# Optimization experiments

Hardware: AMD Instinct MI355X
Metric: run time of the kernel (lower is better)

## Reference

```python
import jax, jax.numpy as jnp
import numpy as np

V, B, NP, NJ = 5, 32, 20, 17
NB = 16
ND = 128
POSE_MIN_DEPTH, POSE_MAX_DEPTH = 2000.0, 8000.0
POSE_SIGMA = 100.0
KS = 11
HIDDEN_ROUGH, HIDDEN = 1024, 1024
BONES = np.array([[0,1],[0,2],[1,3],[2,4],[5,6],[5,7],[7,9],[6,8],[8,10],[5,11],[6,12],[11,12],[11,13],[13,15],[12,14],[14,16]], dtype=np.int32)


def setup_inputs() -> dict:
    key = jax.random.key(0)
    ks = jax.random.split(key, 12)
    wh = jnp.array([1920.0, 1080.0], jnp.float32)
    kpts = jax.random.uniform(ks[0], (V, B, NP, NJ, 2), jnp.float32) * wh
    pose_vis = jnp.ones((V, B, NP), jnp.float32)
    joint_vis = (jax.random.uniform(ks[1], (V, B, NP, NJ)) > 0.15).astype(jnp.float32)
    gt_pose_depths = jax.random.uniform(ks[2], (B, NP), jnp.float32, 2000.0, 8000.0)
    gt_joint_depths = jax.random.uniform(ks[3], (B, NP, NJ), jnp.float32, -100.0, 100.0)
    angles = np.linspace(-0.3, 0.3, V)
    Rs = np.stack([np.array([[np.cos(a), 0.0, np.sin(a)], [0.0, 1.0, 0.0], [-np.sin(a), 0.0, np.cos(a)]], dtype=np.float32) for a in angles])
    cam_R = jnp.broadcast_to(jnp.asarray(Rs)[:, None], (V, B, 3, 3))
    tvec = np.zeros((V, 3), np.float32); tvec[:, 0] = np.linspace(-500.0, 500.0, V)
    cam_T = jnp.broadcast_to(jnp.asarray(tvec)[:, None], (V, B, 3))
    cam_f = jnp.full((V, B, 2), 1400.0, jnp.float32)
    cam_c = jnp.broadcast_to(jnp.array([960.0, 540.0], jnp.float32), (V, B, 2))
    image_wh = jnp.broadcast_to(jnp.array([1920.0, 1080.0], jnp.float32), (V, B, 2))
    num_persons = jax.random.randint(ks[4], (V, B), 10, NP + 1, jnp.int32)
    Wr1 = jax.random.normal(ks[5], (HIDDEN_ROUGH, NJ * 2)) * 0.02
    br1 = jnp.zeros((HIDDEN_ROUGH,), jnp.float32)
    Wr2 = jax.random.normal(ks[6], (NJ, HIDDEN_ROUGH)) * 0.02
    br2 = jnp.zeros((NJ,), jnp.float32)
    Wc1 = jax.random.normal(ks[7], (HIDDEN, NJ + NB, 3)) * 0.02
    bc1 = jnp.zeros((HIDDEN,), jnp.float32)
    Wc2 = jax.random.normal(ks[8], (1, HIDDEN, 3)) * 0.02
    bc2 = jnp.zeros((1,), jnp.float32)
    bones = jnp.asarray(BONES)
    return dict(kpts=kpts, pose_vis=pose_vis, joint_vis=joint_vis, gt_pose_depths=gt_pose_depths, gt_joint_depths=gt_joint_depths, cam_R=cam_R, cam_T=cam_T, cam_f=cam_f, cam_c=cam_c, image_wh=image_wh, num_persons=num_persons, Wr1=Wr1, br1=br1, Wr2=Wr2, br2=br2, Wc1=Wc1, bc1=bc1, Wc2=Wc2, bc2=bc2, bones=bones)


def _bone_len(p, bones):
    # p: [B, Np, Nj, D, 2] -> [B, Np, Nb, D]
    a = p[:, :, bones[:, 0]]
    b = p[:, :, bones[:, 1]]
    return jnp.sqrt(jnp.sum((a - b) ** 2, -1) + 1e-12)


def _conv1d(x, w, b):
    # x [N,C,L], w [O,I,3]
    y = jax.lax.conv_general_dilated(x, w, (1,), 'SAME', dimension_numbers=('NCH', 'OIH', 'NCH'))
    return y + b[None, :, None]


def _forward(kpts, joint_vis, cam_R, cam_T, cam_f, cam_c, image_wh, num_persons, Wr1, br1, Wr2, br2, Wc1, bc1, Wc2, bc2, bones):
    V_, B_, NP_, NJ_, _ = kpts.shape
    labels = jnp.arange(ND, dtype=jnp.float32) / (ND - 1) * (POSE_MAX_DEPTH - POSE_MIN_DEPTH) + POSE_MIN_DEPTH
    kt = kpts[0]  # target-view 2D poses [B,Np,Nj,2]
    # faithful to original indexing quirk: normalize all batches by batch-0 image size
    kn = kt / image_wh[0, 0][None, None, None, :]
    x = kn.reshape(B_ * NP_, NJ_ * 2)
    h = jax.nn.relu(x @ Wr1.T + br1)
    rough = (h @ Wr2.T + br2).reshape(B_, NP_, NJ_) * 1000.0
    rough = jax.lax.stop_gradient(rough)  # .detach() in original
    depths = labels[None, None, None, :] + rough[..., None]  # [B,Np,Nj,D]
    # back-project target 2D poses at every depth hypothesis
    R0, T0, f0, c0 = cam_R[0], cam_T[0], cam_f[0], cam_c[0]
    uvn = (kt - c0[:, None, None, :]) / f0[:, None, None, :]
    xy = uvn[..., None, :] * depths[..., None]
    cam_pts = jnp.concatenate([xy, depths[..., None]], -1)
    p3d = jnp.einsum('bji,bpkdj->bpkdi', R0, cam_pts) + T0[:, None, None, None, :]  # world [B,Np,Nj,D,3]

    scores = scores2 = boundings = boundings2 = None
    for rv in range(1, V_):
        Rr, Tr, fr, cr = cam_R[rv], cam_T[rv], cam_f[rv], cam_c[rv]
        xc = jnp.einsum('bij,bpkdj->bpkdi', Rr, p3d - Tr[:, None, None, None, :])
        p2t = xc[..., :2] / (xc[..., 2:3] + 1e-8) * fr[:, None, None, None, :] + cr[:, None, None, None, :]
        pr = kpts[rv]         # [B,Npr,Nj,2]
        vr = joint_vis[rv]    # [B,Npr,Nj]
        # pairwise dist over (target-person, ref-person) per joint/depth
        d = jnp.sum((p2t[:, :, None] - pr[:, None, :, :, None, :]) ** 2, -1)  # [B,Npt,Npr,Nj,D]
        w = vr[:, None, :, :, None]
        pdist = jnp.sum(d * w, 3) / (jnp.sum(w, 3) + 1e-8)  # [B,Npt,Npr,D]
        valid = jnp.arange(NP_)[None, None, :, None] < num_persons[rv][:, None, None, None]
        pdist = jnp.where(valid, pdist, 1e5)
        mm = jnp.argmin(pdist, 2)  # [B,Npt,D] nearest ref pose
        bidx = jnp.arange(B_)[:, None, None]
        matched = jnp.transpose(pr[bidx, mm], (0, 1, 3, 2, 4))  # [B,Npt,Nj,D,2]
        mvis = jnp.transpose(vr[bidx, mm], (0, 1, 3, 2))        # [B,Npt,Nj,D]
        mdist = jnp.sum((p2t - matched) ** 2, -1)
        score = jnp.exp(-jnp.sqrt(mdist + 1e-12) / POSE_SIGMA)  # panoptic branch
        score_bl = jnp.exp(-jnp.abs(_bone_len(matched, bones) - _bone_len(p2t, bones)) / 5.0)
        wimg = image_wh[rv][:, None, None, None, 0]
        himg = image_wh[rv][:, None, None, None, 1]
        inb = ((p2t[..., 0] >= 0) & (p2t[..., 1] >= 0) & (p2t[..., 0] <= wimg - 1) & (p2t[..., 1] <= himg - 1)).astype(score.dtype)
        bounding = inb * mvis
        bounding2 = jnp.broadcast_to(mvis[:, :, :1, :], score_bl.shape)
        if scores is None:
            scores, scores2 = score * bounding, score_bl * bounding2
            boundings, boundings2 = bounding, bounding2
        else:
            scores = scores + score * bounding
            scores2 = scores2 + score_bl * bounding2
            boundings = boundings + bounding
            boundings2 = boundings2 + bounding2
    psv = (scores / (boundings + 1e-8)).reshape(B_ * NP_, NJ_, ND)
    psv2 = (scores2 / (boundings2 + 1e-8)).reshape(B_ * NP_, NB, ND)
    xin = jnp.concatenate([psv, psv2], 1)  # [BN, Nj+Nb, D]
    hc = jax.nn.relu(_conv1d(xin, Wc1, bc1))
    logits = _conv1d(hc, Wc2, bc2)[:, 0, :]  # [BN, D]
    vol = jax.nn.softmax(logits, -1)
    # soft-argmax restricted to a window around the argmax
    pos = jnp.arange(ND, dtype=vol.dtype)
    idx = jnp.argmax(vol, -1)
    mask = (jnp.abs(pos[None, :] - idx[:, None].astype(vol.dtype)) <= KS // 2).astype(vol.dtype)
    mv = vol * mask
    mv = mv / (jnp.sum(mv, -1, keepdims=True) + 1e-8)
    pred_idx = jnp.sum(mv * pos, -1).reshape(B_, NP_)
    return pred_idx / (ND - 1) * (POSE_MAX_DEPTH - POSE_MIN_DEPTH) + POSE_MIN_DEPTH


def reference(kpts, pose_vis, joint_vis, gt_pose_depths, gt_joint_depths, cam_R, cam_T, cam_f, cam_c, image_wh, num_persons, Wr1, br1, Wr2, br2, Wc1, bc1, Wc2, bc2, bones):
    return _forward(kpts, joint_vis, cam_R, cam_T, cam_f, cam_c, image_wh, num_persons, Wr1, br1, Wr2, br2, Wc1, bc1, Wc2, bc2, bones)
```

## Files before the change

kernel.cpp:

```cpp
#include <hip/hip_runtime.h>
#include <math.h>

#define VV  5
#define BB  32
#define NPP 20
#define NJJ 17
#define NBB 16
#define NDD 128
#define HID 1024
#define KPITCH 128
#define KSTEPS 7
#define PRP 36
#define VRP 20

typedef __attribute__((ext_vector_type(8))) short short8;
typedef __attribute__((ext_vector_type(16))) float float16;

static constexpr int BONE_A[NBB] = {0,0,1,2,5,5,7,6,8,5,6,11,11,13,12,14};
static constexpr int BONE_B[NBB] = {1,2,3,4,6,7,9,8,10,11,12,12,13,15,14,16};

__device__ __forceinline__ float warp_red_sum(float v) {
#pragma unroll
  for (int off = 32; off >= 1; off >>= 1) v += __shfl_xor(v, off, 64);
  return v;
}

__global__ __launch_bounds__(256) void prep_kernel(
    const float* __restrict__ Wc1, unsigned short* __restrict__ A_hi,
    unsigned short* __restrict__ A_lo) {
  int idx = blockIdx.x * 256 + threadIdx.x;
  int o = idx >> 7, kk = idx & 127;
  float x = (kk < 99) ? Wc1[o * 99 + kk] : 0.0f;
  unsigned int u = __float_as_uint(x);
  unsigned short hi = (unsigned short)(u >> 16);
  float xh = __uint_as_float((u >> 16) << 16);
  float r = x - xh;
  unsigned short lo = (unsigned short)(__float_as_uint(r) >> 16);
  A_hi[idx] = hi;
  A_lo[idx] = lo;
}

__global__ __launch_bounds__(512, 8) void pose_front_kernel(
    const float* __restrict__ kpts, const float* __restrict__ joint_vis,
    const float* __restrict__ cam_R, const float* __restrict__ cam_T,
    const float* __restrict__ cam_f, const float* __restrict__ cam_c,
    const float* __restrict__ image_wh, const int* __restrict__ num_persons,
    const float* __restrict__ Wr1, const float* __restrict__ br1,
    const float* __restrict__ Wr2, const float* __restrict__ br2,
    float* __restrict__ ws_xin) {
  const int n = blockIdx.x;
  const int b = n / NPP;
  const int p = n % NPP;
  const int tid = threadIdx.x;
  const int wv = tid >> 6, ln = tid & 63;
  const int rvv = tid >> 7;
  const int d   = tid & (NDD - 1);

  __shared__ float sh_x[NJJ * 2];
  __shared__ float sh_h[HID];
  __shared__ float sh_rough[NJJ];
  __shared__ float sh_base[NJJ][3];
  __shared__ __align__(16) float sh_pr[4][NPP][PRP];
  __shared__ __align__(16) float sh_vr[4][NPP][VRP];
  __shared__ float sh_stage[4][8][NDD];
  __shared__ float sh_s2red[NBB][NDD];

  if (tid < NJJ * 2) {
    int j = tid >> 1, c = tid & 1;
    float k = kpts[((size_t)(b * NPP + p)) * NJJ * 2 + j * 2 + c];
    sh_x[tid] = k / image_wh[c];
  }
  __syncthreads();

#pragma unroll
  for (int k = 0; k < 2; ++k) {
    int m = tid + k * 512;
    float acc = br1[m];
#pragma unroll
    for (int c = 0; c < NJJ * 2; ++c) acc = fmaf(Wr1[m * (NJJ * 2) + c], sh_x[c], acc);
    sh_h[m] = fmaxf(acc, 0.0f);
  }
  __syncthreads();

  for (int j = wv; j < NJJ; j += 8) {
    float part = 0.0f;
    for (int m = ln; m < HID; m += 64) part = fmaf(Wr2[j * HID + m], sh_h[m], part);
    part = warp_red_sum(part);
    if (ln == 0) sh_rough[j] = (part + br2[j]) * 1000.0f;
  }
  if (tid < NJJ) {
    int j = tid;
    const float* R0 = cam_R + (size_t)b * 9;
    float c0x = cam_c[b * 2 + 0], c0y = cam_c[b * 2 + 1];
    float f0x = cam_f[b * 2 + 0], f0y = cam_f[b * 2 + 1];
    float kx = kpts[((size_t)(b * NPP + p)) * NJJ * 2 + j * 2 + 0];
    float ky = kpts[((size_t)(b * NPP + p)) * NJJ * 2 + j * 2 + 1];
    float ux = (kx - c0x) / f0x;
    float uy = (ky - c0y) / f0y;
#pragma unroll
    for (int i = 0; i < 3; ++i)
      sh_base[j][i] = R0[0 * 3 + i] * ux + R0[1 * 3 + i] * uy + R0[2 * 3 + i];
  }
#pragma unroll
  for (int rr = 0; rr < 4; ++rr) {
    const float* prg = kpts + ((size_t)(rr + 1) * BB + b) * NPP * NJJ * 2;
    for (int idx = tid; idx < NPP * NJJ * 2; idx += 512)
      sh_pr[rr][idx / 34][idx % 34] = prg[idx];
    const float* vrg = joint_vis + ((size_t)(rr + 1) * BB + b) * NPP * NJJ;
    for (int idx = tid; idx < NPP * NJJ; idx += 512)
      sh_vr[rr][idx / 17][idx % 17] = vrg[idx];
  }
  if (tid < 4 * BB) {
    int rr = tid >> 5, q = tid & 31;
    if (q < NPP) {
      sh_pr[rr][q][34] = 0.0f; sh_pr[rr][q][35] = 0.0f;
      sh_vr[rr][q][17] = 0.0f; sh_vr[rr][q][18] = 0.0f; sh_vr[rr][q][19] = 0.0f;
    }
  }
  __syncthreads();

  float partA[NJJ];
  float partS[NBB];
  unsigned int maskB;
  float partb2;
  {
    const int rv = rvv + 1;
    const int vb = rv * BB + b;
    const float* Rr = cam_R + (size_t)vb * 9;
    const float R00 = Rr[0], R01 = Rr[1], R02 = Rr[2];
    const float R10 = Rr[3], R11 = Rr[4], R12 = Rr[5];
    const float R20 = Rr[6], R21 = Rr[7], R22 = Rr[8];
    const float Trx = cam_T[vb * 3 + 0], Try = cam_T[vb * 3 + 1], Trz = cam_T[vb * 3 + 2];
    const float frx = cam_f[vb * 2 + 0], fry = cam_f[vb * 2 + 1];
    const float crx = cam_c[vb * 2 + 0], cry = cam_c[vb * 2 + 1];
    const float wmax = image_wh[vb * 2 + 0] - 1.0f;
    const float hmax = image_wh[vb * 2 + 1] - 1.0f;
    const int nprv = num_persons[vb];
    const float T0x = cam_T[b * 3 + 0], T0y = cam_T[b * 3 + 1], T0z = cam_T[b * 3 + 2];
    const float lab = ((float)d / 127.0f) * 6000.0f + 2000.0f;

    float px[NJJ], py[NJJ];
#pragma unroll
    for (int j = 0; j < NJJ; ++j) {
      float dep = lab + sh_rough[j];
      float p0 = fmaf(dep, sh_base[j][0], T0x);
      float p1 = fmaf(dep, sh_base[j][1], T0y);
      float p2 = fmaf(dep, sh_base[j][2], T0z);
      float q0 = p0 - Trx, q1 = p1 - Try, q2 = p2 - Trz;
      float xc0 = R00 * q0 + R01 * q1 + R02 * q2;
      float xc1 = R10 * q0 + R11 * q1 + R12 * q2;
      float xc2 = R20 * q0 + R21 * q1 + R22 * q2 + 1e-8f;
      px[j] = xc0 / xc2 * frx + crx;
      py[j] = xc1 / xc2 * fry + cry;
    }

    float best = 3.4e38f;
    int mm = 0;
#pragma unroll 1
    for (int q = 0; q < NPP; ++q) {
      const float4* pr4 = (const float4*)(&sh_pr[rvv][q][0]);
      const float4* vr4 = (const float4*)(&sh_vr[rvv][q][0]);
      float num = 0.0f, den = 0.0f;
#pragma unroll
      for (int g4 = 0; g4 < 4; ++g4) {
        float4 w  = vr4[g4];
        float4 pa = pr4[2 * g4 + 0];
        float4 pb = pr4[2 * g4 + 1];
        { float dx = px[4*g4+0] - pa.x, dy = py[4*g4+0] - pa.y; num = fmaf(w.x, dx*dx + dy*dy, num); den += w.x; }
        { float dx = px[4*g4+1] - pa.z, dy = py[4*g4+1] - pa.w; num = fmaf(w.y, dx*dx + dy*dy, num); den += w.y; }
        { float dx = px[4*g4+2] - pb.x, dy = py[4*g4+2] - pb.y; num = fmaf(w.z, dx*dx + dy*dy, num); den += w.z; }
        { float dx = px[4*g4+3] - pb.z, dy = py[4*g4+3] - pb.w; num = fmaf(w.w, dx*dx + dy*dy, num); den += w.w; }
      }
      {
        float w16 = sh_vr[rvv][q][16];
        float4 pc = pr4[8];
        float dx = px[16] - pc.x, dy = py[16] - pc.y;
        num = fmaf(w16, dx*dx + dy*dy, num); den += w16;
      }
      float pd = num / (den + 1e-8f);
      if (q >= nprv) pd = 100000.0f;
      if (pd < best) { best = pd; mm = q; }
    }

    maskB = 0u;
#pragma unroll
    for (int j = 0; j < NJJ; ++j) {
      float mx = sh_pr[rvv][mm][j * 2 + 0];
      float my = sh_pr[rvv][mm][j * 2 + 1];
      float mv = sh_vr[rvv][mm][j];
      float dx = px[j] - mx, dy = py[j] - my;
      float sc = expf(-sqrtf(dx * dx + dy * dy + 1e-12f) / 100.0f);
      float inb = (px[j] >= 0.0f && py[j] >= 0.0f && px[j] <= wmax && py[j] <= hmax) ? 1.0f : 0.0f;
      float bd = inb * mv;
      partA[j] = sc * bd;
      maskB |= ((unsigned int)(bd != 0.0f)) << j;
    }
    float v0 = sh_vr[rvv][mm][0];
#pragma unroll
    for (int nb = 0; nb < NBB; ++nb) {
      const int a = BONE_A[nb], c = BONE_B[nb];
      float ax = sh_pr[rvv][mm][a * 2 + 0], ay = sh_pr[rvv][mm][a * 2 + 1];
      float cx = sh_pr[rvv][mm][c * 2 + 0], cy = sh_pr[rvv][mm][c * 2 + 1];
      float dmx = ax - cx, dmy = ay - cy;
      float blm = sqrtf(dmx * dmx + dmy * dmy + 1e-12f);
      float dpx = px[a] - px[c], dpy = py[a] - py[c];
      float blp = sqrtf(dpx * dpx + dpy * dpy + 1e-12f);
      float scb = expf(-fabsf(blm - blp) / 5.0f);
      partS[nb] = scb * v0;
    }
    partb2 = v0;
  }

  float* xo = ws_xin + (size_t)n * (NJJ + NBB) * NDD;
#pragma unroll
  for (int r = 0; r < 7; ++r) {
#pragma unroll
    for (int i = 0; i < 8; ++i) {
      const int ch = r * 8 + i;
      if (ch <= 50) {
        float v;
        if (ch < 34) v = (ch & 1) ? (float)((maskB >> (ch >> 1)) & 1u) : partA[ch >> 1];
        else if (ch < 50) v = partS[ch - 34];
        else v = partb2;
        sh_stage[rvv][i][d] = v;
      }
    }
    __syncthreads();
    if (tid < NDD) {
      float sjv = 0.0f;
#pragma unroll
      for (int i = 0; i < 8; ++i) {
        const int ch = r * 8 + i;
        if (ch > 50) continue;
        float s = ((sh_stage[0][i][tid] + sh_stage[1][i][tid]) + sh_stage[2][i][tid]) + sh_stage[3][i][tid];
        if (ch < 34) {
          if ((ch & 1) == 0) sjv = s;
          else xo[(ch >> 1) * NDD + tid] = sjv / (s + 1e-8f);
        } else if (ch < 50) {
          sh_s2red[ch - 34][tid] = s;
        } else {
          float den2 = s + 1e-8f;
#pragma unroll
          for (int nb = 0; nb < NBB; ++nb)
            xo[(NJJ + nb) * NDD + tid] = sh_s2red[nb][tid] / den2;
        }
      }
    }
    __syncthreads();
  }
}

__global__ __launch_bounds__(512, 2) void conv_mfma_kernel(
    const float* __restrict__ ws_xin,
    const unsigned short* __restrict__ A_hi, const unsigned short* __restrict__ A_lo,
    const float* __restrict__ bc1, const float* __restrict__ Wc2,
    const float* __restrict__ bc2, float* __restrict__ out) {
  const int n = blockIdx.x;
  const int tid = threadIdx.x;
  const int w = tid >> 6;
  const int l = tid & 63;
  const int lrow = l & 31;
  const int g = l >> 5;

  __shared__ __align__(16) unsigned short bT_hi[128 * KPITCH];
  __shared__ __align__(16) unsigned short bT_lo[128 * KPITCH];
  __shared__ float plg[3][8][NDD];
  __shared__ float sh_l[NDD];
  __shared__ float sh_e[NDD];
  __shared__ float sh_sc[2];

  for (int i = tid; i < 3 * 8 * NDD; i += 512) ((float*)plg)[i] = 0.0f;

  const float* xn = ws_xin + (size_t)n * (NJJ + NBB) * NDD;
  for (int idx = tid; idx < 64 * 128; idx += 512) {
    const int kp = (idx & 63) << 1;
    const int t  = idx >> 6;
    unsigned int hp = 0, lp = 0;
#pragma unroll
    for (int u = 0; u < 2; ++u) {
      const int kk = kp + u;
      float x = 0.0f;
      if (kk < 99) {
        int i3 = kk / 3;
        int k3 = kk - i3 * 3;
        int tt = t + k3 - 1;
        if (tt >= 0 && tt < 128) x = xn[i3 * NDD + tt];
      }
      unsigned int uu = __float_as_uint(x);
      unsigned int hi = uu >> 16;
      float xh = __uint_as_float(hi << 16);
      unsigned int lo = __float_as_uint(x - xh) >> 16;
      hp |= hi << (16 * u);
      lp |= lo << (16 * u);
    }
    const int e = t * KPITCH + (kp ^ ((t & 15) << 3));
    *(unsigned int*)(bT_hi + e) = hp;
    *(unsigned int*)(bT_lo + e) = lp;
  }
  __syncthreads();

#pragma unroll 1
  for (int otile = 0; otile < 4; ++otile) {
    const int o0 = w * 128 + otile * 32;

    short8 Ah[KSTEPS], Al[KSTEPS];
    {
      const unsigned short* arh = A_hi + (size_t)(o0 + lrow) * KPITCH + g * 8;
      const unsigned short* arl = A_lo + (size_t)(o0 + lrow) * KPITCH + g * 8;
#pragma unroll
      for (int ks = 0; ks < KSTEPS; ++ks) {
        Ah[ks] = *(const short8*)(arh + ks * 16);
        Al[ks] = *(const short8*)(arl + ks * 16);
      }
    }

#pragma unroll 1
    for (int ttile = 0; ttile < 4; ++ttile) {
      const int trow = ttile * 32 + lrow;
      const unsigned short* brh = bT_hi + trow * KPITCH;
      const unsigned short* brl = bT_lo + trow * KPITCH;
      const int sw = (trow & 15) << 3;

      float16 X, Y;
#pragma unroll
      for (int r = 0; r < 16; ++r) { X[r] = 0.0f; Y[r] = 0.0f; }

#pragma unroll
      for (int ks = 0; ks < KSTEPS; ++ks) {
        const int e = (ks * 16 + g * 8) ^ sw;
        short8 bh = *(const short8*)(brh + e);
        X = __builtin_amdgcn_mfma_f32_32x32x16_bf16(Ah[ks], bh, X, 0, 0, 0);
        Y = __builtin_amdgcn_mfma_f32_32x32x16_bf16(Al[ks], bh, Y, 0, 0, 0);
      }
#pragma unroll
      for (int ks = 0; ks < KSTEPS; ++ks) {
        const int e = (ks * 16 + g * 8) ^ sw;
        short8 bl = *(const short8*)(brl + e);
        if (ks & 1) Y = __builtin_amdgcn_mfma_f32_32x32x16_bf16(Ah[ks], bl, Y, 0, 0, 0);
        else        X = __builtin_amdgcn_mfma_f32_32x32x16_bf16(Ah[ks], bl, X, 0, 0, 0);
      }

      float sP = 0.0f, sC = 0.0f, sM = 0.0f;
#pragma unroll
      for (int r = 0; r < 16; ++r) {
        const int orow = o0 + 4 * g + 8 * (r >> 2) + (r & 3);
        float h = fmaxf((X[r] + Y[r]) + bc1[orow], 0.0f);
        sP = fmaf(h, Wc2[orow * 3 + 0], sP);
        sC = fmaf(h, Wc2[orow * 3 + 1], sC);
        sM = fmaf(h, Wc2[orow * 3 + 2], sM);
      }
      sP += __shfl_xor(sP, 32, 64);
      sC += __shfl_xor(sC, 32, 64);
      sM += __shfl_xor(sM, 32, 64);
      if (l < 32) {
        plg[0][w][trow] += sP;
        plg[1][w][trow] += sC;
        plg[2][w][trow] += sM;
      }
    }
  }
  __syncthreads();

  if (tid < NDD) {
    int t = tid;
    float lg = bc2[0];
#pragma unroll
    for (int ww = 0; ww < 8; ++ww) lg += plg[1][ww][t];
    if (t > 0) {
#pragma unroll
      for (int ww = 0; ww < 8; ++ww) lg += plg[0][ww][t - 1];
    }
    if (t < NDD - 1) {
#pragma unroll
      for (int ww = 0; ww < 8; ++ww) lg += plg[2][ww][t + 1];
    }
    sh_l[t] = lg;
  }
  __syncthreads();
  if (tid < 64) {
    float v1 = sh_l[tid], v2 = sh_l[tid + 64];
    float mv; int mi;
    if (v2 > v1) { mv = v2; mi = tid + 64; } else { mv = v1; mi = tid; }
#pragma unroll
    for (int off = 32; off >= 1; off >>= 1) {
      float ov = __shfl_xor(mv, off, 64);
      int   oi = __shfl_xor(mi, off, 64);
      if (ov > mv || (ov == mv && oi < mi)) { mv = ov; mi = oi; }
    }
    if (tid == 0) { sh_sc[0] = mv; ((int*)sh_sc)[1] = mi; }
  }
  __syncthreads();
  const float gmax = sh_sc[0];
  const int gidx = ((const int*)sh_sc)[1];
  if (tid < NDD) sh_e[tid] = expf(sh_l[tid] - gmax);
  __syncthreads();
  if (tid < 64) {
    float S = warp_red_sum(sh_e[tid] + sh_e[tid + 64]);
    float a1 = 0.0f, a2 = 0.0f;
#pragma unroll
    for (int k = 0; k < 2; ++k) {
      int t = tid + k * 64;
      float vol = sh_e[t] / S;
      float msk = (fabsf((float)t - (float)gidx) <= 5.0f) ? 1.0f : 0.0f;
      float mvv = vol * msk;
      a1 += mvv;
      a2 += mvv * (float)t;
    }
    a1 = warp_red_sum(a1);
    a2 = warp_red_sum(a2);
    if (tid == 0) {
      float pred = a2 / (a1 + 1e-8f);
      out[n] = pred / 127.0f * 6000.0f + 2000.0f;
    }
  }
}

extern "C" void kernel_launch(void* const* d_in, const int* in_sizes, int n_in,
                              void* d_out, int out_size, void* d_ws, size_t ws_size,
                              hipStream_t stream) {
  (void)in_sizes; (void)n_in; (void)out_size; (void)ws_size;
  const float* kpts        = (const float*)d_in[0];
  const float* joint_vis   = (const float*)d_in[2];
  const float* cam_R       = (const float*)d_in[5];
  const float* cam_T       = (const float*)d_in[6];
  const float* cam_f       = (const float*)d_in[7];
  const float* cam_c       = (const float*)d_in[8];
  const float* image_wh    = (const float*)d_in[9];
  const int*   num_persons = (const int*)d_in[10];
  const float* Wr1 = (const float*)d_in[11];
  const float* br1 = (const float*)d_in[12];
  const float* Wr2 = (const float*)d_in[13];
  const float* br2 = (const float*)d_in[14];
  const float* Wc1 = (const float*)d_in[15];
  const float* bc1 = (const float*)d_in[16];
  const float* Wc2 = (const float*)d_in[17];
  const float* bc2 = (const float*)d_in[18];
  float* out = (float*)d_out;

  unsigned short* A_hi = (unsigned short*)d_ws;
  unsigned short* A_lo = A_hi + HID * KPITCH;
  float* ws_xin = (float*)(A_lo + HID * KPITCH);

  hipLaunchKernelGGL(prep_kernel, dim3((HID * KPITCH) / 256), dim3(256), 0, stream,
                     Wc1, A_hi, A_lo);
  hipLaunchKernelGGL(pose_front_kernel, dim3(BB * NPP), dim3(512), 0, stream,
                     kpts, joint_vis, cam_R, cam_T, cam_f, cam_c, image_wh,
                     num_persons, Wr1, br1, Wr2, br2, ws_xin);
  hipLaunchKernelGGL(conv_mfma_kernel, dim3(BB * NPP), dim3(512), 0, stream,
                     ws_xin, A_hi, A_lo, bc1, Wc2, bc2, out);
}
```

Before: 192.3 us.

## Move cross-view reduction into separate kernel and hoist conv epilogue weights

```diff
diff --git a/kernel.cpp b/kernel.cpp
--- a/kernel.cpp
+++ b/kernel.cpp
@@ -12,6 +12,7 @@
 #define KSTEPS 7
 #define PRP 36
 #define VRP 20
+#define NCH 34
 
 typedef __attribute__((ext_vector_type(8))) short short8;
 typedef __attribute__((ext_vector_type(16))) float float16;
@@ -47,7 +48,7 @@
     const float* __restrict__ image_wh, const int* __restrict__ num_persons,
     const float* __restrict__ Wr1, const float* __restrict__ br1,
     const float* __restrict__ Wr2, const float* __restrict__ br2,
-    float* __restrict__ ws_xin) {
+    float* __restrict__ ws_partial) {
   const int n = blockIdx.x;
   const int b = n / NPP;
   const int p = n % NPP;
@@ -62,8 +63,6 @@
   __shared__ float sh_base[NJJ][3];
   __shared__ __align__(16) float sh_pr[4][NPP][PRP];
   __shared__ __align__(16) float sh_vr[4][NPP][VRP];
-  __shared__ float sh_stage[4][8][NDD];
-  __shared__ float sh_s2red[NBB][NDD];
 
   if (tid < NJJ * 2) {
     int j = tid >> 1, c = tid & 1;
@@ -119,10 +118,6 @@
   }
   __syncthreads();
 
-  float partA[NJJ];
-  float partS[NBB];
-  unsigned int maskB;
-  float partb2;
   {
     const int rv = rvv + 1;
     const int vb = rv * BB + b;
@@ -182,7 +177,8 @@
       if (pd < best) { best = pd; mm = q; }
     }
 
-    maskB = 0u;
+    float* pbase = ws_partial + (((size_t)n * NCH) * 4 + rvv) * 128 + d;
+    unsigned int maskB = 0u;
 #pragma unroll
     for (int j = 0; j < NJJ; ++j) {
       float mx = sh_pr[rvv][mm][j * 2 + 0];
@@ -192,10 +188,11 @@
       float sc = expf(-sqrtf(dx * dx + dy * dy + 1e-12f) / 100.0f);
       float inb = (px[j] >= 0.0f && py[j] >= 0.0f && px[j] <= wmax && py[j] <= hmax) ? 1.0f : 0.0f;
       float bd = inb * mv;
-      partA[j] = sc * bd;
+      pbase[j * 512] = sc * bd;
       maskB |= ((unsigned int)(bd != 0.0f)) << j;
     }
     float v0 = sh_vr[rvv][mm][0];
+    maskB |= ((unsigned int)(v0 != 0.0f)) << 17;
 #pragma unroll
     for (int nb = 0; nb < NBB; ++nb) {
       const int a = BONE_A[nb], c = BONE_B[nb];
@@ -206,47 +203,38 @@
       float dpx = px[a] - px[c], dpy = py[a] - py[c];
       float blp = sqrtf(dpx * dpx + dpy * dpy + 1e-12f);
       float scb = expf(-fabsf(blm - blp) / 5.0f);
-      partS[nb] = scb * v0;
-    }
-    partb2 = v0;
-  }
-
+      pbase[(NJJ + nb) * 512] = scb * v0;
+    }
+    *(unsigned int*)(pbase + 33 * 512) = maskB;
+  }
+}
+
+__global__ __launch_bounds__(128) void reduce_kernel(
+    const float* __restrict__ ws_partial, float* __restrict__ ws_xin) {
+  const int n = blockIdx.x;
+  const int t = threadIdx.x;
+  const float* pb = ws_partial + ((size_t)n * NCH) * 4 * 128;
   float* xo = ws_xin + (size_t)n * (NJJ + NBB) * NDD;
-#pragma unroll
-  for (int r = 0; r < 7; ++r) {
-#pragma unroll
-    for (int i = 0; i < 8; ++i) {
-      const int ch = r * 8 + i;
-      if (ch <= 50) {
-        float v;
-        if (ch < 34) v = (ch & 1) ? (float)((maskB >> (ch >> 1)) & 1u) : partA[ch >> 1];
-        else if (ch < 50) v = partS[ch - 34];
-        else v = partb2;
-        sh_stage[rvv][i][d] = v;
-      }
-    }
-    __syncthreads();
-    if (tid < NDD) {
-      float sjv = 0.0f;
-#pragma unroll
-      for (int i = 0; i < 8; ++i) {
-        const int ch = r * 8 + i;
-        if (ch > 50) continue;
-        float s = ((sh_stage[0][i][tid] + sh_stage[1][i][tid]) + sh_stage[2][i][tid]) + sh_stage[3][i][tid];
-        if (ch < 34) {
-          if ((ch & 1) == 0) sjv = s;
-          else xo[(ch >> 1) * NDD + tid] = sjv / (s + 1e-8f);
-        } else if (ch < 50) {
-          sh_s2red[ch - 34][tid] = s;
-        } else {
-          float den2 = s + 1e-8f;
-#pragma unroll
-          for (int nb = 0; nb < NBB; ++nb)
-            xo[(NJJ + nb) * NDD + tid] = sh_s2red[nb][tid] / den2;
-        }
-      }
-    }
-    __syncthreads();
+
+  unsigned int m0 = __float_as_uint(pb[(33 * 4 + 0) * 128 + t]);
+  unsigned int m1 = __float_as_uint(pb[(33 * 4 + 1) * 128 + t]);
+  unsigned int m2 = __float_as_uint(pb[(33 * 4 + 2) * 128 + t]);
+  unsigned int m3 = __float_as_uint(pb[(33 * 4 + 3) * 128 + t]);
+
+#pragma unroll
+  for (int i = 0; i < NJJ; ++i) {
+    const float* a = pb + (i * 4) * 128 + t;
+    float s = ((a[0] + a[128]) + a[256]) + a[384];
+    int bj = ((m0 >> i) & 1) + ((m1 >> i) & 1) + ((m2 >> i) & 1) + ((m3 >> i) & 1);
+    xo[i * NDD + t] = s / ((float)bj + 1e-8f);
+  }
+  int b2 = ((m0 >> 17) & 1) + ((m1 >> 17) & 1) + ((m2 >> 17) & 1) + ((m3 >> 17) & 1);
+  float den2 = (float)b2 + 1e-8f;
+#pragma unroll
+  for (int nb = 0; nb < NBB; ++nb) {
+    const float* a = pb + ((NJJ + nb) * 4) * 128 + t;
+    float s = ((a[0] + a[128]) + a[256]) + a[384];
+    xo[(NJJ + nb) * NDD + t] = s / den2;
   }
 }
 
@@ -313,6 +301,22 @@
         Al[ks] = *(const short8*)(arl + ks * 16);
       }
     }
+    float w2f[48];
+    float bcf[16];
+#pragma unroll
+    for (int rb = 0; rb < 4; ++rb) {
+      int base = o0 + 4 * g + 8 * rb;
+      float4 wa = *(const float4*)(Wc2 + base * 3 + 0);
+      float4 wb = *(const float4*)(Wc2 + base * 3 + 4);
+      float4 wc = *(const float4*)(Wc2 + base * 3 + 8);
+      w2f[rb * 12 + 0] = wa.x;  w2f[rb * 12 + 1] = wa.y;  w2f[rb * 12 + 2] = wa.z;
+      w2f[rb * 12 + 3] = wa.w;  w2f[rb * 12 + 4] = wb.x;  w2f[rb * 12 + 5] = wb.y;
+      w2f[rb * 12 + 6] = wb.z;  w2f[rb * 12 + 7] = wb.w;  w2f[rb * 12 + 8] = wc.x;
+      w2f[rb * 12 + 9] = wc.y;  w2f[rb * 12 + 10] = wc.z; w2f[rb * 12 + 11] = wc.w;
+      float4 bb = *(const float4*)(bc1 + base);
+      bcf[rb * 4 + 0] = bb.x; bcf[rb * 4 + 1] = bb.y;
+      bcf[rb * 4 + 2] = bb.z; bcf[rb * 4 + 3] = bb.w;
+    }
 
 #pragma unroll 1
     for (int ttile = 0; ttile < 4; ++ttile) {
@@ -343,11 +347,10 @@
       float sP = 0.0f, sC = 0.0f, sM = 0.0f;
 #pragma unroll
       for (int r = 0; r < 16; ++r) {
-        const int orow = o0 + 4 * g + 8 * (r >> 2) + (r & 3);
-        float h = fmaxf((X[r] + Y[r]) + bc1[orow], 0.0f);
-        sP = fmaf(h, Wc2[orow * 3 + 0], sP);
-        sC = fmaf(h, Wc2[orow * 3 + 1], sC);
-        sM = fmaf(h, Wc2[orow * 3 + 2], sM);
+        float h = fmaxf((X[r] + Y[r]) + bcf[(r >> 2) * 4 + (r & 3)], 0.0f);
+        sP = fmaf(h, w2f[(r >> 2) * 12 + (r & 3) * 3 + 0], sP);
+        sC = fmaf(h, w2f[(r >> 2) * 12 + (r & 3) * 3 + 1], sC);
+        sM = fmaf(h, w2f[(r >> 2) * 12 + (r & 3) * 3 + 2], sM);
       }
       sP += __shfl_xor(sP, 32, 64);
       sC += __shfl_xor(sC, 32, 64);
@@ -439,13 +442,16 @@
 
   unsigned short* A_hi = (unsigned short*)d_ws;
   unsigned short* A_lo = A_hi + HID * KPITCH;
-  float* ws_xin = (float*)(A_lo + HID * KPITCH);
+  float* ws_xin     = (float*)(A_lo + HID * KPITCH);
+  float* ws_partial = ws_xin + (size_t)BB * NPP * (NJJ + NBB) * NDD;
 
   hipLaunchKernelGGL(prep_kernel, dim3((HID * KPITCH) / 256), dim3(256), 0, stream,
                      Wc1, A_hi, A_lo);
   hipLaunchKernelGGL(pose_front_kernel, dim3(BB * NPP), dim3(512), 0, stream,
                      kpts, joint_vis, cam_R, cam_T, cam_f, cam_c, image_wh,
-                     num_persons, Wr1, br1, Wr2, br2, ws_xin);
+                     num_persons, Wr1, br1, Wr2, br2, ws_partial);
+  hipLaunchKernelGGL(reduce_kernel, dim3(BB * NPP), dim3(128), 0, stream,
+                     ws_partial, ws_xin);
   hipLaunchKernelGGL(conv_mfma_kernel, dim3(BB * NPP), dim3(512), 0, stream,
                      ws_xin, A_hi, A_lo, bc1, Wc2, bc2, out);
 }
```

New measurement: 190.6 us. No clear change (-0.9%).
